# Kernel tuning notes

Measured on AMD Instinct MI355X. Metric: run time of the kernel, lower is better.

The kernel has to match this reference:

```python
import jax, jax.numpy as jnp
import numpy as np

N_NODES = 50000
N_EDGES = 1600000
IN_CH = 128
HEADS = 4
OUT_CH = 32
NEG_SLOPE = 0.2
EPS = 1e-9


def setup_inputs() -> dict:
    key = jax.random.key(0)
    k_x, k_ei, k_w, k_as, k_ad = jax.random.split(key, 5)
    x = jax.random.normal(k_x, (N_NODES, IN_CH), dtype=jnp.float32)
    edge_index = jax.random.randint(k_ei, (2, N_EDGES), 0, N_NODES, dtype=jnp.int64)
    # xavier-uniform-like init for params
    wb = np.sqrt(6.0 / (IN_CH + HEADS * OUT_CH))
    weight = jax.random.uniform(k_w, (IN_CH, HEADS * OUT_CH), minval=-wb, maxval=wb, dtype=jnp.float32)
    ab = np.sqrt(6.0 / (HEADS + OUT_CH))
    att_src = jax.random.uniform(k_as, (HEADS, OUT_CH), minval=-ab, maxval=ab, dtype=jnp.float32)
    att_dst = jax.random.uniform(k_ad, (HEADS, OUT_CH), minval=-ab, maxval=ab, dtype=jnp.float32)
    bias = jnp.zeros((HEADS * OUT_CH,), dtype=jnp.float32)
    return {"x": x, "edge_index": edge_index, "weight": weight,
            "att_src": att_src, "att_dst": att_dst, "bias": bias}


def reference(x, edge_index, weight, att_src, att_dst, bias):
    N = x.shape[0]
    H, C = att_src.shape
    # add self loops
    loop = jnp.arange(N, dtype=edge_index.dtype)
    ei = jnp.concatenate([edge_index, jnp.stack([loop, loop], axis=0)], axis=1)
    src, dst = ei[0], ei[1]
    # linear projection -> [N, H, C]
    h = (x @ weight).reshape(N, H, C)
    # per-node attention logits, then gather per edge (same math as gathering h first)
    a_s = jnp.einsum('nhc,hc->nh', h, att_src)  # [N, H]
    a_d = jnp.einsum('nhc,hc->nh', h, att_dst)  # [N, H]
    scores = a_s[src] + a_d[dst]                # [E, H]
    scores = jnp.where(scores >= 0, scores, NEG_SLOPE * scores)  # leaky_relu
    # edge softmax over incoming edges of each dst node (all heads vectorized)
    mx = jax.ops.segment_max(scores, dst, num_segments=N)        # [N, H]
    ex = jnp.exp(scores - mx[dst])                               # [E, H]
    denom = jax.ops.segment_sum(ex, dst, num_segments=N)         # [N, H]
    alpha = ex / (denom[dst] + EPS)                              # [E, H]
    # weighted scatter-add aggregation
    msgs = alpha[:, :, None] * h[src]                            # [E, H, C]
    agg = jax.ops.segment_sum(msgs, dst, num_segments=N)         # [N, H, C]
    out = agg.reshape(N, H * C) + bias
    return out
```

## Files before the change

kernel.cpp:

```cpp
#include <hip/hip_runtime.h>

#define NN 50000
#define NE 1600000
#define IN_CH 128
#define HEADS 4
#define OUT_CH 32
#define HC 128
#define NEG_SLOPE 0.2f
#define EPS 1e-9f
#define SEG 96
#define CSTR 8

#define FGRP 8
#define DPG (NN / FGRP)
#define FILL_BPG ((NE / 8 + 255) / 256)
#define ROWS_PB 64
#define PROJ_BLOCKS ((NN + ROWS_PB - 1) / ROWS_PB)
#define XPITCH 136
#define INIT_BLOCKS ((NN + 255) / 256)
#define GMAX_BLOCKS ((NN + 255) / 256)

#define ENC_NEG_INF 0x007FFFFFu

using bf16x8 = __attribute__((ext_vector_type(8))) short;
using f32x4  = __attribute__((ext_vector_type(4))) float;
using u16x8  = __attribute__((ext_vector_type(8))) unsigned short;

__device__ __forceinline__ float leaky(float v) {
    return v >= 0.0f ? v : NEG_SLOPE * v;
}
__device__ __forceinline__ unsigned short f2bf(float f) {
    unsigned u = __float_as_uint(f);
    return (unsigned short)((u + 0x7fffu + ((u >> 16) & 1u)) >> 16);
}
__device__ __forceinline__ float bf2f(unsigned short b) {
    return __uint_as_float((unsigned)b << 16);
}
__device__ __forceinline__ unsigned int fenc(float f) {
    unsigned int u = __float_as_uint(f);
    return (u & 0x80000000u) ? ~u : (u | 0x80000000u);
}
__device__ __forceinline__ float fdec(unsigned int u) {
    return (u & 0x80000000u) ? __uint_as_float(u & 0x7fffffffu)
                             : __uint_as_float(~u);
}

__global__ __launch_bounds__(256) void k_init(int* __restrict__ cnt,
                                              unsigned int* __restrict__ gmax,
                                              const float* __restrict__ W,
                                              unsigned short* __restrict__ Wt_bf) {
    const int i = blockIdx.x * 256 + threadIdx.x;
    if (i < HEADS) gmax[i] = ENC_NEG_INF;
    if (i < NN) {
        const int4 z = make_int4(0, 0, 0, 0);
        *(int4*)(cnt + (size_t)i * CSTR) = z;
        *(int4*)(cnt + (size_t)i * CSTR + 4) = z;
    }
    if (i < IN_CH * HC) {
        int k = i >> 7, n = i & 127;
        Wt_bf[n * IN_CH + k] = f2bf(W[i]);
    }
}

__global__ __launch_bounds__(256) void k_proj_fill(
        const float* __restrict__ x,
        const unsigned short* __restrict__ Wt_bf,
        const float* __restrict__ att_s, const float* __restrict__ att_d,
        unsigned short* __restrict__ h_bf,
        float* __restrict__ a_s, float* __restrict__ a_d,
        const int* __restrict__ ei, int* __restrict__ cnt,
        unsigned short* __restrict__ csr_src) {
    if (blockIdx.x >= PROJ_BLOCKS) {
        const int fb = blockIdx.x - PROJ_BLOCKS;
        const int f = fb & (FGRP - 1);
        const int bg = fb >> 3;
        const int e0 = (bg * 256 + (int)threadIdx.x) * 8;
        if (e0 >= NE) return;
        const int lo = f * DPG;
        const int4 d0 = *(const int4*)(ei + NE + e0);
        const int4 d1 = *(const int4*)(ei + NE + e0 + 4);
        const int4 s0 = *(const int4*)(ei + e0);
        const int4 s1 = *(const int4*)(ei + e0 + 4);
        const int d[8] = {d0.x, d0.y, d0.z, d0.w, d1.x, d1.y, d1.z, d1.w};
        const int s[8] = {s0.x, s0.y, s0.z, s0.w, s1.x, s1.y, s1.z, s1.w};
#pragma unroll
        for (int k = 0; k < 8; ++k) {
            if ((unsigned)(d[k] - lo) < (unsigned)DPG) {
                const int pos = atomicAdd(&cnt[(size_t)d[k] * CSTR], 1);
                if (pos < SEG)
                    csr_src[(size_t)d[k] * SEG + pos] = (unsigned short)s[k];
            }
        }
        return;
    }
    __shared__ short xs[ROWS_PB * XPITCH];
    const int tid = threadIdx.x;
    const int n0 = blockIdx.x * ROWS_PB;

#pragma unroll
    for (int it = 0; it < 8; ++it) {
        const int idx = it * 256 + tid;
        const int row = idx >> 5;
        const int k4 = idx & 31;
        float4 v = make_float4(0.f, 0.f, 0.f, 0.f);
        if (n0 + row < NN) v = *(const float4*)(x + (size_t)(n0 + row) * IN_CH + k4 * 4);
        short* p = &xs[row * XPITCH + k4 * 4];
        p[0] = (short)f2bf(v.x); p[1] = (short)f2bf(v.y);
        p[2] = (short)f2bf(v.z); p[3] = (short)f2bf(v.w);
    }
    __syncthreads();

    const int wave = tid >> 6;
    const int lane = tid & 63;
    const int quad = lane >> 4;
    const int m16 = lane & 15;
    const int wrow = wave * 16;

    bf16x8 a[4];
#pragma unroll
    for (int ks = 0; ks < 4; ++ks)
        a[ks] = *(const bf16x8*)&xs[(wrow + m16) * XPITCH + ks * 32 + quad * 8];

    const int row_base = n0 + wrow + quad * 4;
#pragma unroll
    for (int hh = 0; hh < 4; ++hh) {
        float psh[4] = {0.f, 0.f, 0.f, 0.f};
        float pdh[4] = {0.f, 0.f, 0.f, 0.f};
#pragma unroll
        for (int c2 = 0; c2 < 2; ++c2) {
            const int ct = hh * 2 + c2;
            const unsigned short* wb = Wt_bf + (size_t)(ct * 16 + m16) * IN_CH + quad * 8;
            bf16x8 b0 = *(const bf16x8*)(wb);
            bf16x8 b1 = *(const bf16x8*)(wb + 32);
            bf16x8 b2 = *(const bf16x8*)(wb + 64);
            bf16x8 b3 = *(const bf16x8*)(wb + 96);
            f32x4 acc = {0.f, 0.f, 0.f, 0.f};
            acc = __builtin_amdgcn_mfma_f32_16x16x32_bf16(a[0], b0, acc, 0, 0, 0);
            acc = __builtin_amdgcn_mfma_f32_16x16x32_bf16(a[1], b1, acc, 0, 0, 0);
            acc = __builtin_amdgcn_mfma_f32_16x16x32_bf16(a[2], b2, acc, 0, 0, 0);
            acc = __builtin_amdgcn_mfma_f32_16x16x32_bf16(a[3], b3, acc, 0, 0, 0);
            const int col = ct * 16 + m16;
            const float asv = att_s[col];
            const float adv = att_d[col];
#pragma unroll
            for (int r = 0; r < 4; ++r) {
                const int n = row_base + r;
                if (n < NN) h_bf[(size_t)n * HC + col] = f2bf(acc[r]);
                psh[r] = fmaf(acc[r], asv, psh[r]);
                pdh[r] = fmaf(acc[r], adv, pdh[r]);
            }
        }
#pragma unroll
        for (int mk = 1; mk <= 8; mk <<= 1) {
#pragma unroll
            for (int r = 0; r < 4; ++r) {
                psh[r] += __shfl_xor(psh[r], mk, 64);
                pdh[r] += __shfl_xor(pdh[r], mk, 64);
            }
        }
        if (m16 == 0) {
#pragma unroll
            for (int r = 0; r < 4; ++r) {
                const int n = row_base + r;
                if (n < NN) {
                    a_s[n * HEADS + hh] = psh[r];
                    a_d[n * HEADS + hh] = pdh[r];
                }
            }
        }
    }
}

__global__ __launch_bounds__(256) void k_gmax(const float* __restrict__ a_s,
                                              const int* __restrict__ cnt,
                                              int* __restrict__ cnt_p,
                                              unsigned int* __restrict__ gmax) {
    const int n = blockIdx.x * 256 + threadIdx.x;
    float4 m4 = make_float4(-1e30f, -1e30f, -1e30f, -1e30f);
    if (n < NN) {
        m4 = *(const float4*)(a_s + n * 4);
        int c = cnt[(size_t)n * CSTR];
        cnt_p[n] = c > SEG ? SEG : c;
    }
#pragma unroll
    for (int m = 32; m >= 1; m >>= 1) {
        m4.x = fmaxf(m4.x, __shfl_xor(m4.x, m, 64));
        m4.y = fmaxf(m4.y, __shfl_xor(m4.y, m, 64));
        m4.z = fmaxf(m4.z, __shfl_xor(m4.z, m, 64));
        m4.w = fmaxf(m4.w, __shfl_xor(m4.w, m, 64));
    }
    __shared__ float wm[4][4];
    const int wv = threadIdx.x >> 6;
    if ((threadIdx.x & 63) == 0) {
        wm[wv][0] = m4.x; wm[wv][1] = m4.y; wm[wv][2] = m4.z; wm[wv][3] = m4.w;
    }
    __syncthreads();
    if (threadIdx.x < 4) {
        float mm = fmaxf(fmaxf(wm[0][threadIdx.x], wm[1][threadIdx.x]),
                         fmaxf(wm[2][threadIdx.x], wm[3][threadIdx.x]));
        atomicMax(&gmax[threadIdx.x], fenc(mm));
    }
}

__global__ __launch_bounds__(256) void k_agg(const int* __restrict__ cnt_p,
                                             const unsigned short* __restrict__ csr_src,
                                             const unsigned short* __restrict__ h_bf,
                                             const float* __restrict__ a_s,
                                             const float* __restrict__ a_d,
                                             const unsigned int* __restrict__ gmax,
                                             const float* __restrict__ bias,
                                             float* __restrict__ out) {
    const int n = blockIdx.x * 4 + (threadIdx.x >> 6);
    const int lane = threadIdx.x & 63;
    if (n >= NN) return;
    const int q = lane >> 4;
    const int ql = lane & 15;
    const int hd = ql >> 2;
    const int dg = cnt_p[n];
    const int beg = n * SEG;
    const int end = beg + dg;

    const float ad_h = a_d[n * 4 + hd];
    const float bound = leaky(fdec(gmax[hd]) + ad_h);

    float ev = 0.25f * __expf(leaky(a_s[n * 4 + hd] + ad_h) - bound);
    float denom = ev;
    const u16x8 hs = *(const u16x8*)(h_bf + (size_t)n * HC + 8 * ql);
    float acc[8];
#pragma unroll
    for (int k = 0; k < 8; ++k) acc[k] = ev * bf2f(hs[k]);

    int i = beg + q;
    int s0v = (i < end)     ? (int)csr_src[i]     : n;
    int s1v = (i + 4 < end) ? (int)csr_src[i + 4] : n;
    float as0 = a_s[s0v * 4 + hd];
    u16x8 hv0 = *(const u16x8*)(h_bf + (size_t)s0v * HC + 8 * ql);

    for (; i < end; i += 4) {
        const int s2v = (i + 8 < end) ? (int)csr_src[i + 8] : n;
        const float as1 = a_s[s1v * 4 + hd];
        const u16x8 hv1 = *(const u16x8*)(h_bf + (size_t)s1v * HC + 8 * ql);
        const float e = __expf(leaky(as0 + ad_h) - bound);
        denom += e;
#pragma unroll
        for (int k = 0; k < 8; ++k)
            acc[k] = fmaf(e, bf2f(hv0[k]), acc[k]);
        as0 = as1; hv0 = hv1; s1v = s2v;
    }
#pragma unroll
    for (int k = 0; k < 8; ++k) {
        acc[k] += __shfl_xor(acc[k], 16, 64);
        acc[k] += __shfl_xor(acc[k], 32, 64);
    }
    denom += __shfl_xor(denom, 16, 64);
    denom += __shfl_xor(denom, 32, 64);

    if (q == 0) {
        const float inv = 1.0f / (denom + EPS);
        float* o = out + (size_t)n * HC + 8 * ql;
        const float* b = bias + 8 * ql;
        f32x4 o0, o1;
        o0[0] = acc[0] * inv + b[0]; o0[1] = acc[1] * inv + b[1];
        o0[2] = acc[2] * inv + b[2]; o0[3] = acc[3] * inv + b[3];
        o1[0] = acc[4] * inv + b[4]; o1[1] = acc[5] * inv + b[5];
        o1[2] = acc[6] * inv + b[6]; o1[3] = acc[7] * inv + b[7];
        __builtin_nontemporal_store(o0, (f32x4*)(o));
        __builtin_nontemporal_store(o1, (f32x4*)(o + 4));
    }
}

extern "C" void kernel_launch(void* const* d_in, const int* in_sizes, int n_in,
                              void* d_out, int out_size, void* d_ws, size_t ws_size,
                              hipStream_t stream) {
    const float* x     = (const float*)d_in[0];
    const int*   ei    = (const int*)d_in[1];
    const float* W     = (const float*)d_in[2];
    const float* att_s = (const float*)d_in[3];
    const float* att_d = (const float*)d_in[4];
    const float* bias  = (const float*)d_in[5];
    float* out = (float*)d_out;

    char* ws = (char*)d_ws;
    int*   cnt     = (int*)ws;    ws += (size_t)NN * CSTR * 4;
    int*   cnt_p   = (int*)ws;    ws += (size_t)NN * 4;
    unsigned int* gmax = (unsigned int*)ws; ws += 64;
    unsigned short* csr_src = (unsigned short*)ws; ws += (size_t)NN * SEG * 2;
    unsigned short* h_bf = (unsigned short*)ws; ws += (size_t)NN * HC * 2;
    float* a_s     = (float*)ws;  ws += (size_t)NN * HEADS * 4;
    float* a_d     = (float*)ws;  ws += (size_t)NN * HEADS * 4;
    unsigned short* Wt_bf = (unsigned short*)ws; ws += (size_t)IN_CH * HC * 2;

    k_init     <<<INIT_BLOCKS, 256, 0, stream>>>(cnt, gmax, W, Wt_bf);
    k_proj_fill<<<PROJ_BLOCKS + FGRP * FILL_BPG, 256, 0, stream>>>(
        x, Wt_bf, att_s, att_d, h_bf, a_s, a_d, ei, cnt, csr_src);
    k_gmax     <<<GMAX_BLOCKS, 256, 0, stream>>>(a_s, cnt, cnt_p, gmax);
    k_agg      <<<(NN + 3) / 4, 256, 0, stream>>>(cnt_p, csr_src, h_bf, a_s, a_d,
                                                  gmax, bias, out);
}
```

Before: 213.9 us.

## Store h head-major and map aggregation blocks per head for XCD L2 locality

The projection now writes h as four per-head slabs of N×32 bf16 instead of node-major rows. The aggregation kernel assigns each block a single head and half of the nodes, ordered so that round-robin dispatch sends each head's gathers to the same XCD, keeping that head's slab resident in that XCD's L2. Each wave processes 8 edges in parallel with 4-channel loads. In exchange, CSR indices and a_s are re-read once per head and the gather loads become narrower.

```diff
diff --git a/kernel.cpp b/kernel.cpp
--- a/kernel.cpp
+++ b/kernel.cpp
@@ -19,12 +19,13 @@
 #define XPITCH 136
 #define INIT_BLOCKS ((NN + 255) / 256)
 #define GMAX_BLOCKS ((NN + 255) / 256)
+#define AGG_BLOCKS 50000
 
 #define ENC_NEG_INF 0x007FFFFFu
 
 using bf16x8 = __attribute__((ext_vector_type(8))) short;
 using f32x4  = __attribute__((ext_vector_type(4))) float;
-using u16x8  = __attribute__((ext_vector_type(8))) unsigned short;
+using u16x4  = __attribute__((ext_vector_type(4))) unsigned short;
 
 __device__ __forceinline__ float leaky(float v) {
     return v >= 0.0f ? v : NEG_SLOPE * v;
@@ -140,12 +141,14 @@
             acc = __builtin_amdgcn_mfma_f32_16x16x32_bf16(a[2], b2, acc, 0, 0, 0);
             acc = __builtin_amdgcn_mfma_f32_16x16x32_bf16(a[3], b3, acc, 0, 0, 0);
             const int col = ct * 16 + m16;
+            const int cc = c2 * 16 + m16;
             const float asv = att_s[col];
             const float adv = att_d[col];
 #pragma unroll
             for (int r = 0; r < 4; ++r) {
                 const int n = row_base + r;
-                if (n < NN) h_bf[(size_t)n * HC + col] = f2bf(acc[r]);
+                if (n < NN)
+                    h_bf[((size_t)hh * NN + n) * 32 + cc] = f2bf(acc[r]);
                 psh[r] = fmaf(acc[r], asv, psh[r]);
                 pdh[r] = fmaf(acc[r], adv, pdh[r]);
             }
@@ -210,12 +213,17 @@
                                              const unsigned int* __restrict__ gmax,
                                              const float* __restrict__ bias,
                                              float* __restrict__ out) {
-    const int n = blockIdx.x * 4 + (threadIdx.x >> 6);
+    const int b = blockIdx.x;
+    const int xc = b & 7;
+    const int j = b >> 3;
+    const int hd = xc >> 1;
+    const int half = xc & 1;
+    const int n = (half * 6250 + j) * 4 + (int)(threadIdx.x >> 6);
     const int lane = threadIdx.x & 63;
-    if (n >= NN) return;
-    const int q = lane >> 4;
-    const int ql = lane & 15;
-    const int hd = ql >> 2;
+    const int eg = lane >> 3;
+    const int cl = lane & 7;
+    const unsigned short* __restrict__ hslab = h_bf + (size_t)hd * NN * 32;
+
     const int dg = cnt_p[n];
     const int beg = n * SEG;
     const int end = beg + dg;
@@ -223,49 +231,48 @@
     const float ad_h = a_d[n * 4 + hd];
     const float bound = leaky(fdec(gmax[hd]) + ad_h);
 
-    float ev = 0.25f * __expf(leaky(a_s[n * 4 + hd] + ad_h) - bound);
+    float ev = 0.125f * __expf(leaky(a_s[n * 4 + hd] + ad_h) - bound);
     float denom = ev;
-    const u16x8 hs = *(const u16x8*)(h_bf + (size_t)n * HC + 8 * ql);
-    float acc[8];
-#pragma unroll
-    for (int k = 0; k < 8; ++k) acc[k] = ev * bf2f(hs[k]);
-
-    int i = beg + q;
+    const u16x4 hs = *(const u16x4*)(hslab + (size_t)n * 32 + 4 * cl);
+    float acc[4];
+#pragma unroll
+    for (int k = 0; k < 4; ++k) acc[k] = ev * bf2f(hs[k]);
+
+    int i = beg + eg;
     int s0v = (i < end)     ? (int)csr_src[i]     : n;
-    int s1v = (i + 4 < end) ? (int)csr_src[i + 4] : n;
+    int s1v = (i + 8 < end) ? (int)csr_src[i + 8] : n;
     float as0 = a_s[s0v * 4 + hd];
-    u16x8 hv0 = *(const u16x8*)(h_bf + (size_t)s0v * HC + 8 * ql);
-
-    for (; i < end; i += 4) {
-        const int s2v = (i + 8 < end) ? (int)csr_src[i + 8] : n;
+    u16x4 hv0 = *(const u16x4*)(hslab + (size_t)s0v * 32 + 4 * cl);
+
+    for (; i < end; i += 8) {
+        const int s2v = (i + 16 < end) ? (int)csr_src[i + 16] : n;
         const float as1 = a_s[s1v * 4 + hd];
-        const u16x8 hv1 = *(const u16x8*)(h_bf + (size_t)s1v * HC + 8 * ql);
+        const u16x4 hv1 = *(const u16x4*)(hslab + (size_t)s1v * 32 + 4 * cl);
         const float e = __expf(leaky(as0 + ad_h) - bound);
         denom += e;
 #pragma unroll
-        for (int k = 0; k < 8; ++k)
+        for (int k = 0; k < 4; ++k)
             acc[k] = fmaf(e, bf2f(hv0[k]), acc[k]);
         as0 = as1; hv0 = hv1; s1v = s2v;
     }
 #pragma unroll
-    for (int k = 0; k < 8; ++k) {
+    for (int k = 0; k < 4; ++k) {
+        acc[k] += __shfl_xor(acc[k], 8, 64);
         acc[k] += __shfl_xor(acc[k], 16, 64);
         acc[k] += __shfl_xor(acc[k], 32, 64);
     }
+    denom += __shfl_xor(denom, 8, 64);
     denom += __shfl_xor(denom, 16, 64);
     denom += __shfl_xor(denom, 32, 64);
 
-    if (q == 0) {
+    if (eg == 0) {
         const float inv = 1.0f / (denom + EPS);
-        float* o = out + (size_t)n * HC + 8 * ql;
-        const float* b = bias + 8 * ql;
-        f32x4 o0, o1;
-        o0[0] = acc[0] * inv + b[0]; o0[1] = acc[1] * inv + b[1];
-        o0[2] = acc[2] * inv + b[2]; o0[3] = acc[3] * inv + b[3];
-        o1[0] = acc[4] * inv + b[4]; o1[1] = acc[5] * inv + b[5];
-        o1[2] = acc[6] * inv + b[6]; o1[3] = acc[7] * inv + b[7];
-        __builtin_nontemporal_store(o0, (f32x4*)(o));
-        __builtin_nontemporal_store(o1, (f32x4*)(o + 4));
+        float* o = out + (size_t)n * HC + hd * 32 + 4 * cl;
+        const float* bb = bias + hd * 32 + 4 * cl;
+        f32x4 ov;
+        ov[0] = acc[0] * inv + bb[0]; ov[1] = acc[1] * inv + bb[1];
+        ov[2] = acc[2] * inv + bb[2]; ov[3] = acc[3] * inv + bb[3];
+        __builtin_nontemporal_store(ov, (f32x4*)o);
     }
 }
 
@@ -294,6 +301,6 @@
     k_proj_fill<<<PROJ_BLOCKS + FGRP * FILL_BPG, 256, 0, stream>>>(
         x, Wt_bf, att_s, att_d, h_bf, a_s, a_d, ei, cnt, csr_src);
     k_gmax     <<<GMAX_BLOCKS, 256, 0, stream>>>(a_s, cnt, cnt_p, gmax);
-    k_agg      <<<(NN + 3) / 4, 256, 0, stream>>>(cnt_p, csr_src, h_bf, a_s, a_d,
-                                                  gmax, bias, out);
-}
+    k_agg      <<<AGG_BLOCKS, 256, 0, stream>>>(cnt_p, csr_src, h_bf, a_s, a_d,
+                                                gmax, bias, out);
+}
```

New measurement: 249.7 us. 16.7% more time.
